# Kernel optimization log

Hardware: AMD Instinct MI355X
Metric: run time of the kernel (lower is better)

The kernel has to match this reference:

```python
import jax, jax.numpy as jnp
import numpy as np

D_MODEL = 1024
DEPTH = 1024

def setup_inputs() -> dict:
    key = jax.random.key(0)
    ks = jax.random.split(key, 7)
    scale = 1.0 / np.sqrt(D_MODEL)
    x = jax.random.normal(ks[0], (4, 2048, D_MODEL), dtype=jnp.float32)
    Wq = jax.random.normal(ks[1], (D_MODEL, DEPTH), dtype=jnp.float32) * scale
    Wk = jax.random.normal(ks[2], (D_MODEL, DEPTH), dtype=jnp.float32) * scale
    Wv = jax.random.normal(ks[3], (D_MODEL, DEPTH), dtype=jnp.float32) * scale
    bq = jnp.zeros((DEPTH,), dtype=jnp.float32)
    bk = jnp.zeros((DEPTH,), dtype=jnp.float32)
    bv = jnp.zeros((DEPTH,), dtype=jnp.float32)
    return {"x": x, "Wq": Wq, "bq": bq, "Wk": Wk, "bk": bk, "Wv": Wv, "bv": bv}

def reference(x, Wq, bq, Wk, bk, Wv, bv):
    # Q/K/V linear projections (Keras Dense: x @ W + b)
    q = jnp.einsum('bsd,de->bse', x, Wq) + bq  # [B,S,depth]
    k = jnp.einsum('bsd,de->bse', x, Wk) + bk
    v = jnp.einsum('bsd,de->bse', x, Wv) + bv
    d_k = jnp.asarray(q.shape[-1], dtype=q.dtype)
    scores = jnp.einsum('bse,bte->bst', q, k) / jnp.sqrt(d_k)  # [B,S,S]
    attn = jax.nn.softmax(scores, axis=-1)
    return jnp.einsum('bst,bte->bse', attn, v)  # [B,S,depth]
```

## Files before the change

kernel.cpp:

```cpp
#include <hip/hip_runtime.h>
#include <stdint.h>
#include <type_traits>

typedef unsigned short u16;
using short8  = __attribute__((ext_vector_type(8))) short;
using floatx4 = __attribute__((ext_vector_type(4))) float;

#define IC(n) (std::integral_constant<int, (n)>())

__device__ __forceinline__ u16 f2bf(float f) {
    unsigned u = __float_as_uint(f);
    u += 0x7fff + ((u >> 16) & 1);
    return (u16)(u >> 16);
}
__device__ __forceinline__ float bf2f(u16 h) {
    return __uint_as_float(((unsigned)h) << 16);
}

__device__ __forceinline__ void gload_lds16(const void* g, void* l) {
    auto gp = reinterpret_cast<const __attribute__((address_space(1))) unsigned int*>(
        reinterpret_cast<uintptr_t>(g));
    auto lp = reinterpret_cast<__attribute__((address_space(3))) unsigned int*>(
        reinterpret_cast<uintptr_t>(l));
    __builtin_amdgcn_global_load_lds(gp, lp, 16, 0, 0);
}

__global__ __launch_bounds__(256) void cvt_f32_bf16_kernel(
        const float* __restrict__ in, u16* __restrict__ out) {
    long i = ((long)blockIdx.x * 256 + threadIdx.x) * 4;
    float4 v = *(const float4*)(in + i);
    ushort4 o;
    o.x = f2bf(v.x); o.y = f2bf(v.y); o.z = f2bf(v.z); o.w = f2bf(v.w);
    *(ushort4*)(out + i) = o;
}

__global__ __launch_bounds__(256) void wt_kernel(
        const float* __restrict__ W0, const float* __restrict__ W1, const float* __restrict__ W2,
        u16* __restrict__ O0, u16* __restrict__ O1, u16* __restrict__ O2) {
    const float* W = blockIdx.z == 0 ? W0 : blockIdx.z == 1 ? W1 : W2;
    u16* O = blockIdx.z == 0 ? O0 : blockIdx.z == 1 ? O1 : O2;
    __shared__ float t[32][33];
    const int cx = threadIdx.x & 31, ry = threadIdx.x >> 5;
    const int d0 = blockIdx.x * 32, e0 = blockIdx.y * 32;
#pragma unroll
    for (int i = 0; i < 4; i++) t[ry + i * 8][cx] = W[(long)(d0 + ry + i * 8) * 1024 + e0 + cx];
    __syncthreads();
#pragma unroll
    for (int i = 0; i < 4; i++) O[(long)(e0 + ry + i * 8) * 1024 + d0 + cx] = f2bf(t[cx][ry + i * 8]);
}

__global__ __launch_bounds__(256) void vt_kernel(
        const u16* __restrict__ V, u16* __restrict__ Vt) {
    const int b = blockIdx.z;
    const u16* v = V + (long)b * 2048 * 1024;
    u16* o = Vt + (long)b * 1024 * 2048;
    __shared__ u16 t[32][33];
    const int cx = threadIdx.x & 31, ry = threadIdx.x >> 5;
    const int e0 = blockIdx.x * 32, t0 = blockIdx.y * 32;
#pragma unroll
    for (int i = 0; i < 4; i++) t[ry + i * 8][cx] = v[(long)(t0 + ry + i * 8) * 1024 + e0 + cx];
    __syncthreads();
#pragma unroll
    for (int i = 0; i < 4; i++) o[(long)(e0 + ry + i * 8) * 2048 + t0 + cx] = t[cx][ry + i * 8];
}

template <int MODE>
__global__ __launch_bounds__(512) void gemm8_kernel(
        const u16* __restrict__ A, const u16* __restrict__ Bt,
        void* __restrict__ out0, void* __restrict__ out1, void* __restrict__ out2,
        const float* __restrict__ b0, const float* __restrict__ b1, const float* __restrict__ b2,
        int K, int N, long sAb, long sBb, long sCb, float scale)
{
    extern __shared__ u16 lds[];
    const int tid = threadIdx.x, lane = tid & 63, wid = tid >> 6;
    const int wm = wid >> 2, wn = wid & 3;
    const int l15 = lane & 15, hib = (lane >> 4) * 16;

    const int nbx = gridDim.x;
    const int nwg = nbx * gridDim.y;
    int lin = blockIdx.y * nbx + blockIdx.x;
    lin = (lin & 7) * (nwg >> 3) + (lin >> 3);
    const long m0 = (long)(lin / nbx) * 256;
    const long n0 = (long)(lin % nbx) * 256;

    const u16* Ab = A + (long)blockIdx.z * sAb;
    const u16* Bb = Bt + (long)blockIdx.z * sBb;
    const long ldk = K;
    const int NT = K >> 6;

    auto stA = [&](int dbuf, int S, int kt) {
#pragma unroll
        for (int i = 0; i < 2; ++i) {
            const int rl = tid >> 3;
            const int R  = S * 64 + rl;
            const int cb = (tid & 7) * 16;
            const int scb = cb ^ ((R & 7) << 4);
            const u16* src = Ab + (m0 + i * 128 + R) * ldk + (long)kt * 64 + (scb >> 1);
            u16* dst = lds + dbuf * 32768 + i * 8192 + S * 4096 + wid * 512;
            gload_lds16(src, dst);
        }
    };
    auto stB = [&](int dbuf, int NHs, int kt) {
#pragma unroll
        for (int i = 0; i < 2; ++i) {
            const int c = i * 2 + (wid >> 2);
            const int h = c >> 1, rb = (c & 1) * 64;
            const int w = (wid & 3) * 64 + lane;
            const int r32 = w >> 3;
            const int R = rb + NHs * 32 + r32;
            const int cb = (w & 7) * 16;
            const int scb = cb ^ ((R & 7) << 4);
            const u16* src = Bb + (n0 + h * 128 + R) * ldk + (long)kt * 64 + (scb >> 1);
            u16* dst = lds + dbuf * 32768 + 16384 + h * 8192 + (rb + NHs * 32) * 64 + (wid & 3) * 512;
            gload_lds16(src, dst);
        }
    };

    floatx4 acc[8][4] = {};
    short8 afr[4][2], bfr[2][2];

    auto LA = [&](int dbuf, auto MHc) {
        constexpr int MH = decltype(MHc)::value;
        const char* reg = (const char*)(lds + dbuf * 32768 + wm * 8192);
#pragma unroll
        for (int fm = 0; fm < 4; ++fm)
#pragma unroll
            for (int ks = 0; ks < 2; ++ks) {
                const int r = MH * 64 + fm * 16 + l15;
                const int cb = ks * 64 + hib;
                afr[fm][ks] = *(const short8*)(reg + r * 128 + (cb ^ ((r & 7) << 4)));
            }
    };
    auto LB = [&](int dbuf, auto NHc) {
        constexpr int NH = decltype(NHc)::value;
        const char* reg = (const char*)(lds + dbuf * 32768 + 16384 + (wn >> 1) * 8192);
#pragma unroll
        for (int fn = 0; fn < 2; ++fn)
#pragma unroll
            for (int ks = 0; ks < 2; ++ks) {
                const int r = (wn & 1) * 64 + NH * 32 + fn * 16 + l15;
                const int cb = ks * 64 + hib;
                bfr[fn][ks] = *(const short8*)(reg + r * 128 + (cb ^ ((r & 7) << 4)));
            }
    };
    auto MM = [&](auto MHc, auto NHc) {
        constexpr int MH = decltype(MHc)::value;
        constexpr int NH = decltype(NHc)::value;
        __builtin_amdgcn_s_setprio(1);
#pragma unroll
        for (int fm = 0; fm < 4; ++fm)
#pragma unroll
            for (int fn = 0; fn < 2; ++fn)
#pragma unroll
                for (int ks = 0; ks < 2; ++ks)
                    acc[MH * 4 + fm][NH * 2 + fn] = __builtin_amdgcn_mfma_f32_16x16x32_bf16(
                        afr[fm][ks], bfr[fn][ks], acc[MH * 4 + fm][NH * 2 + fn], 0, 0, 0);
        __builtin_amdgcn_s_setprio(0);
    };

#define BAR()   __builtin_amdgcn_s_barrier()
#define WAIT0() asm volatile("s_waitcnt lgkmcnt(0)" ::: "memory")

    stA(0, 0, 0); stA(0, 1, 0); stB(0, 0, 0); stB(0, 1, 0);
    stA(1, 0, 1); stB(1, 1, 1); stA(1, 1, 1);
    asm volatile("s_waitcnt vmcnt(6)");
    BAR();

    auto pair = [&](auto LASTC, int kt0) {
        constexpr bool L = decltype(LASTC)::value;
        LA(0, IC(0)); LB(0, IC(0));
        stB(1, 0, kt0 + 1);
        asm volatile("s_waitcnt lgkmcnt(8)");
        BAR(); WAIT0(); MM(IC(0), IC(0)); BAR();
        LB(0, IC(1));
        if (!L) stA(0, 0, kt0 + 2);
        BAR(); WAIT0(); MM(IC(0), IC(1)); BAR();
        LA(0, IC(1));
        if (!L) stB(0, 1, kt0 + 2);
        BAR(); WAIT0(); MM(IC(1), IC(1)); BAR();
        LB(0, IC(0));
        if (!L) stA(0, 1, kt0 + 2);
        BAR(); WAIT0(); MM(IC(1), IC(0));
        if (L) asm volatile("s_waitcnt vmcnt(0)");
        else   asm volatile("s_waitcnt vmcnt(6)");
        BAR();
        LA(1, IC(0)); LB(1, IC(0));
        if (!L) stB(0, 0, kt0 + 2);
        asm volatile("s_waitcnt lgkmcnt(8)");
        BAR(); WAIT0(); MM(IC(0), IC(0)); BAR();
        LB(1, IC(1));
        if (!L) stA(1, 0, kt0 + 3);
        BAR(); WAIT0(); MM(IC(0), IC(1)); BAR();
        LA(1, IC(1));
        if (!L) stB(1, 1, kt0 + 3);
        BAR(); WAIT0(); MM(IC(1), IC(1)); BAR();
        LB(1, IC(0));
        if (!L) stA(1, 1, kt0 + 3);
        BAR(); WAIT0(); MM(IC(1), IC(0));
        if (L) asm volatile("s_waitcnt vmcnt(0)");
        else   asm volatile("s_waitcnt vmcnt(6)");
        BAR();
    };

    const int NITER = NT >> 1;
    int it = 0;
    for (; it < NITER - 1; ++it) pair(std::false_type{}, 2 * it);
    pair(std::true_type{}, 2 * it);

#undef BAR
#undef WAIT0

    const int cr = (lane >> 4) * 4, cc = l15;
    if (MODE == 0) {
        const int sel = (int)(n0 >> 10);
        u16* O = (u16*)(sel == 0 ? out0 : sel == 1 ? out1 : out2);
        const float* bias = sel == 0 ? b0 : sel == 1 ? b1 : b2;
        const long nc0 = n0 & 1023;
#pragma unroll
        for (int an = 0; an < 4; ++an) {
            const long col = nc0 + wn * 64 + an * 16 + cc;
            const float bvv = bias[col];
#pragma unroll
            for (int am = 0; am < 8; ++am) {
                const long row = m0 + wm * 128 + am * 16 + cr;
#pragma unroll
                for (int j = 0; j < 4; ++j)
                    O[(row + j) * 1024 + col] = f2bf(acc[am][an][j] + bvv);
            }
        }
    } else {
#pragma unroll
        for (int an = 0; an < 4; ++an) {
            const long col = n0 + wn * 64 + an * 16 + cc;
#pragma unroll
            for (int am = 0; am < 8; ++am) {
                const long row = m0 + wm * 128 + am * 16 + cr;
#pragma unroll
                for (int j = 0; j < 4; ++j) {
                    const long idx = (long)blockIdx.z * sCb + (row + j) * (long)N + col;
                    if (MODE == 1) ((u16*)out0)[idx] = f2bf(acc[am][an][j] * scale);
                    else           ((float*)out0)[idx] = acc[am][an][j];
                }
            }
        }
    }
}

__global__ __launch_bounds__(256) void softmax_kernel(u16* __restrict__ S) {
    u16* p = S + (long)blockIdx.x * 2048;
    const int tid = threadIdx.x;
    union { int4 q; u16 u[8]; } in;
    in.q = *(const int4*)(p + tid * 8);
    float v[8];
#pragma unroll
    for (int i = 0; i < 8; i++) v[i] = bf2f(in.u[i]);
    float mx = v[0];
#pragma unroll
    for (int i = 1; i < 8; i++) mx = fmaxf(mx, v[i]);
#pragma unroll
    for (int off = 32; off; off >>= 1) mx = fmaxf(mx, __shfl_xor(mx, off));
    __shared__ float red[8];
    if ((tid & 63) == 0) red[tid >> 6] = mx;
    __syncthreads();
    mx = fmaxf(fmaxf(red[0], red[1]), fmaxf(red[2], red[3]));
    float s = 0.f;
#pragma unroll
    for (int i = 0; i < 8; i++) { v[i] = __expf(v[i] - mx); s += v[i]; }
#pragma unroll
    for (int off = 32; off; off >>= 1) s += __shfl_xor(s, off);
    if ((tid & 63) == 0) red[4 + (tid >> 6)] = s;
    __syncthreads();
    s = red[4] + red[5] + red[6] + red[7];
    const float inv = 1.f / s;
    union { int4 q; u16 u[8]; } out;
#pragma unroll
    for (int i = 0; i < 8; i++) out.u[i] = f2bf(v[i] * inv);
    *(int4*)(p + tid * 8) = out.q;
}

extern "C" void kernel_launch(void* const* d_in, const int* in_sizes, int n_in,
                              void* d_out, int out_size, void* d_ws, size_t ws_size,
                              hipStream_t stream) {
    const float* x  = (const float*)d_in[0];
    const float* Wq = (const float*)d_in[1];
    const float* bq = (const float*)d_in[2];
    const float* Wk = (const float*)d_in[3];
    const float* bk = (const float*)d_in[4];
    const float* Wv = (const float*)d_in[5];
    const float* bv = (const float*)d_in[6];
    float* out = (float*)d_out;

    char* ws = (char*)d_ws;
    const long MB = 1L << 20;
    u16* xb = (u16*)(ws);
    u16* wt = (u16*)(ws + 16 * MB);
    u16* Q  = (u16*)(ws + 22 * MB);
    u16* Kb = (u16*)(ws + 38 * MB);
    u16* Vb = (u16*)(ws + 54 * MB);
    u16* Vt = (u16*)(ws + 70 * MB);
    u16* Sc = (u16*)(ws + 86 * MB);

    (void)hipFuncSetAttribute((const void*)gemm8_kernel<0>, hipFuncAttributeMaxDynamicSharedMemorySize, 131072);
    (void)hipFuncSetAttribute((const void*)gemm8_kernel<1>, hipFuncAttributeMaxDynamicSharedMemorySize, 131072);
    (void)hipFuncSetAttribute((const void*)gemm8_kernel<2>, hipFuncAttributeMaxDynamicSharedMemorySize, 131072);

    cvt_f32_bf16_kernel<<<8192, 256, 0, stream>>>(x, xb);
    wt_kernel<<<dim3(32, 32, 3), 256, 0, stream>>>(Wq, Wk, Wv, wt, wt + 1024 * 1024, wt + 2 * 1024 * 1024);
    gemm8_kernel<0><<<dim3(12, 32, 1), 512, 131072, stream>>>(
        xb, wt, Q, Kb, Vb, bq, bk, bv, 1024, 3072, 0, 0, 0, 1.f);
    vt_kernel<<<dim3(32, 64, 4), 256, 0, stream>>>(Vb, Vt);
    gemm8_kernel<1><<<dim3(8, 8, 4), 512, 131072, stream>>>(
        Q, Kb, Sc, nullptr, nullptr, nullptr, nullptr, nullptr,
        1024, 2048, 2048L * 1024, 2048L * 1024, 2048L * 2048, 0.03125f);
    softmax_kernel<<<8192, 256, 0, stream>>>(Sc);
    gemm8_kernel<2><<<dim3(4, 8, 4), 512, 131072, stream>>>(
        Sc, Vt, out, nullptr, nullptr, nullptr, nullptr, nullptr,
        2048, 1024, 2048L * 2048, 1024L * 2048, 2048L * 1024, 1.f);
}
```

Measured before the change: 198.6 us.

## Shrink GEMM tiles to 128x128, stage epilogue through LDS, vectorize V transpose

The three GEMMs move from 256x256 tiles with a finely interleaved 8-wave schedule to 128x128 tiles with a simpler double-buffered pipeline. LDS use drops to 64KB and the grids get four times as many workgroups. Epilogues now write through a swizzled LDS tile so global stores become 16-byte vectorized rows. The V transpose uses 64x64 tiles with ushort4 accesses. Smaller tiles improve occupancy and wave quantization but lower arithmetic intensity per tile and add global traffic.

```diff
diff --git a/kernel.cpp b/kernel.cpp
--- a/kernel.cpp
+++ b/kernel.cpp
@@ -4,6 +4,7 @@
 
 typedef unsigned short u16;
 using short8  = __attribute__((ext_vector_type(8))) short;
+using ushort8 = __attribute__((ext_vector_type(8))) unsigned short;
 using floatx4 = __attribute__((ext_vector_type(4))) float;
 
 #define IC(n) (std::integral_constant<int, (n)>())
@@ -54,14 +55,21 @@
     const int b = blockIdx.z;
     const u16* v = V + (long)b * 2048 * 1024;
     u16* o = Vt + (long)b * 1024 * 2048;
-    __shared__ u16 t[32][33];
-    const int cx = threadIdx.x & 31, ry = threadIdx.x >> 5;
-    const int e0 = blockIdx.x * 32, t0 = blockIdx.y * 32;
-#pragma unroll
-    for (int i = 0; i < 4; i++) t[ry + i * 8][cx] = v[(long)(t0 + ry + i * 8) * 1024 + e0 + cx];
-    __syncthreads();
-#pragma unroll
-    for (int i = 0; i < 4; i++) o[(long)(e0 + ry + i * 8) * 2048 + t0 + cx] = t[cx][ry + i * 8];
+    __shared__ u16 t[64][68];
+    const int c4 = (threadIdx.x & 15) * 4, r = threadIdx.x >> 4;
+    const int e0 = blockIdx.x * 64, t0 = blockIdx.y * 64;
+#pragma unroll
+    for (int i = 0; i < 4; i++)
+        *(ushort4*)&t[r + i * 16][c4] =
+            *(const ushort4*)(v + (long)(t0 + r + i * 16) * 1024 + e0 + c4);
+    __syncthreads();
+#pragma unroll
+    for (int i = 0; i < 4; i++) {
+        const int e = r + i * 16;
+        ushort4 d;
+        d.x = t[c4 + 0][e]; d.y = t[c4 + 1][e]; d.z = t[c4 + 2][e]; d.w = t[c4 + 3][e];
+        *(ushort4*)(o + (long)(e0 + e) * 2048 + t0 + c4) = d;
+    }
 }
 
 template <int MODE>
@@ -72,133 +80,107 @@
         int K, int N, long sAb, long sBb, long sCb, float scale)
 {
     extern __shared__ u16 lds[];
+    constexpr int DB = 16384;
     const int tid = threadIdx.x, lane = tid & 63, wid = tid >> 6;
-    const int wm = wid >> 2, wn = wid & 3;
+    const int wm = wid >> 1, wn = wid & 1;
     const int l15 = lane & 15, hib = (lane >> 4) * 16;
 
     const int nbx = gridDim.x;
     const int nwg = nbx * gridDim.y;
     int lin = blockIdx.y * nbx + blockIdx.x;
     lin = (lin & 7) * (nwg >> 3) + (lin >> 3);
-    const long m0 = (long)(lin / nbx) * 256;
-    const long n0 = (long)(lin % nbx) * 256;
+    const long m0 = (long)(lin / nbx) * 128;
+    const long n0 = (long)(lin % nbx) * 128;
 
     const u16* Ab = A + (long)blockIdx.z * sAb;
     const u16* Bb = Bt + (long)blockIdx.z * sBb;
     const long ldk = K;
     const int NT = K >> 6;
 
-    auto stA = [&](int dbuf, int S, int kt) {
+    auto stA = [&](int dbuf, int kt) {
 #pragma unroll
         for (int i = 0; i < 2; ++i) {
-            const int rl = tid >> 3;
-            const int R  = S * 64 + rl;
+            const int R  = i * 64 + (tid >> 3);
             const int cb = (tid & 7) * 16;
             const int scb = cb ^ ((R & 7) << 4);
-            const u16* src = Ab + (m0 + i * 128 + R) * ldk + (long)kt * 64 + (scb >> 1);
-            u16* dst = lds + dbuf * 32768 + i * 8192 + S * 4096 + wid * 512;
+            const u16* src = Ab + (m0 + R) * ldk + (long)kt * 64 + (scb >> 1);
+            u16* dst = lds + dbuf * DB + i * 4096 + tid * 8;
             gload_lds16(src, dst);
         }
     };
-    auto stB = [&](int dbuf, int NHs, int kt) {
+    auto stB = [&](int dbuf, int kt) {
 #pragma unroll
         for (int i = 0; i < 2; ++i) {
-            const int c = i * 2 + (wid >> 2);
-            const int h = c >> 1, rb = (c & 1) * 64;
-            const int w = (wid & 3) * 64 + lane;
-            const int r32 = w >> 3;
-            const int R = rb + NHs * 32 + r32;
-            const int cb = (w & 7) * 16;
+            const int R  = i * 64 + (tid >> 3);
+            const int cb = (tid & 7) * 16;
             const int scb = cb ^ ((R & 7) << 4);
-            const u16* src = Bb + (n0 + h * 128 + R) * ldk + (long)kt * 64 + (scb >> 1);
-            u16* dst = lds + dbuf * 32768 + 16384 + h * 8192 + (rb + NHs * 32) * 64 + (wid & 3) * 512;
+            const u16* src = Bb + (n0 + R) * ldk + (long)kt * 64 + (scb >> 1);
+            u16* dst = lds + dbuf * DB + 8192 + i * 4096 + tid * 8;
             gload_lds16(src, dst);
         }
     };
 
-    floatx4 acc[8][4] = {};
-    short8 afr[4][2], bfr[2][2];
-
-    auto LA = [&](int dbuf, auto MHc) {
-        constexpr int MH = decltype(MHc)::value;
-        const char* reg = (const char*)(lds + dbuf * 32768 + wm * 8192);
-#pragma unroll
-        for (int fm = 0; fm < 4; ++fm)
+    floatx4 acc[2][4] = {};
+    short8 a[2][2], b[4][2];
+
+    auto LA = [&](int dbuf) {
+        const char* reg = (const char*)(lds + dbuf * DB);
+#pragma unroll
+        for (int fm = 0; fm < 2; ++fm)
 #pragma unroll
             for (int ks = 0; ks < 2; ++ks) {
-                const int r = MH * 64 + fm * 16 + l15;
+                const int r = wm * 32 + fm * 16 + l15;
                 const int cb = ks * 64 + hib;
-                afr[fm][ks] = *(const short8*)(reg + r * 128 + (cb ^ ((r & 7) << 4)));
-            }
-    };
-    auto LB = [&](int dbuf, auto NHc) {
-        constexpr int NH = decltype(NHc)::value;
-        const char* reg = (const char*)(lds + dbuf * 32768 + 16384 + (wn >> 1) * 8192);
-#pragma unroll
-        for (int fn = 0; fn < 2; ++fn)
+                a[fm][ks] = *(const short8*)(reg + r * 128 + (cb ^ ((r & 7) << 4)));
+            }
+    };
+    auto LB = [&](int dbuf) {
+        const char* reg = (const char*)(lds + dbuf * DB + 8192);
+#pragma unroll
+        for (int fn = 0; fn < 4; ++fn)
 #pragma unroll
             for (int ks = 0; ks < 2; ++ks) {
-                const int r = (wn & 1) * 64 + NH * 32 + fn * 16 + l15;
+                const int r = wn * 64 + fn * 16 + l15;
                 const int cb = ks * 64 + hib;
-                bfr[fn][ks] = *(const short8*)(reg + r * 128 + (cb ^ ((r & 7) << 4)));
-            }
-    };
-    auto MM = [&](auto MHc, auto NHc) {
-        constexpr int MH = decltype(MHc)::value;
-        constexpr int NH = decltype(NHc)::value;
+                b[fn][ks] = *(const short8*)(reg + r * 128 + (cb ^ ((r & 7) << 4)));
+            }
+    };
+    auto MM = [&](auto FMc) {
+        constexpr int FM = decltype(FMc)::value;
         __builtin_amdgcn_s_setprio(1);
 #pragma unroll
-        for (int fm = 0; fm < 4; ++fm)
-#pragma unroll
-            for (int fn = 0; fn < 2; ++fn)
-#pragma unroll
-                for (int ks = 0; ks < 2; ++ks)
-                    acc[MH * 4 + fm][NH * 2 + fn] = __builtin_amdgcn_mfma_f32_16x16x32_bf16(
-                        afr[fm][ks], bfr[fn][ks], acc[MH * 4 + fm][NH * 2 + fn], 0, 0, 0);
+        for (int ks = 0; ks < 2; ++ks)
+#pragma unroll
+            for (int fn = 0; fn < 4; ++fn)
+                acc[FM][fn] = __builtin_amdgcn_mfma_f32_16x16x32_bf16(
+                    a[FM][ks], b[fn][ks], acc[FM][fn], 0, 0, 0);
         __builtin_amdgcn_s_setprio(0);
     };
 
-#define BAR()   __builtin_amdgcn_s_barrier()
-#define WAIT0() asm volatile("s_waitcnt lgkmcnt(0)" ::: "memory")
-
-    stA(0, 0, 0); stA(0, 1, 0); stB(0, 0, 0); stB(0, 1, 0);
-    stA(1, 0, 1); stB(1, 1, 1); stA(1, 1, 1);
-    asm volatile("s_waitcnt vmcnt(6)");
+#define BAR() __builtin_amdgcn_s_barrier()
+
+    stA(0, 0); stB(0, 0);
+    stA(1, 1);
+    asm volatile("s_waitcnt vmcnt(2)");
     BAR();
 
     auto pair = [&](auto LASTC, int kt0) {
         constexpr bool L = decltype(LASTC)::value;
-        LA(0, IC(0)); LB(0, IC(0));
-        stB(1, 0, kt0 + 1);
-        asm volatile("s_waitcnt lgkmcnt(8)");
-        BAR(); WAIT0(); MM(IC(0), IC(0)); BAR();
-        LB(0, IC(1));
-        if (!L) stA(0, 0, kt0 + 2);
-        BAR(); WAIT0(); MM(IC(0), IC(1)); BAR();
-        LA(0, IC(1));
-        if (!L) stB(0, 1, kt0 + 2);
-        BAR(); WAIT0(); MM(IC(1), IC(1)); BAR();
-        LB(0, IC(0));
-        if (!L) stA(0, 1, kt0 + 2);
-        BAR(); WAIT0(); MM(IC(1), IC(0));
+        stB(1, kt0 + 1);
+        LA(0); LB(0);
+        BAR(); MM(IC(0)); BAR();
+        if (!L) stA(0, kt0 + 2);
+        BAR(); MM(IC(1));
         if (L) asm volatile("s_waitcnt vmcnt(0)");
-        else   asm volatile("s_waitcnt vmcnt(6)");
+        else   asm volatile("s_waitcnt vmcnt(2)");
         BAR();
-        LA(1, IC(0)); LB(1, IC(0));
-        if (!L) stB(0, 0, kt0 + 2);
-        asm volatile("s_waitcnt lgkmcnt(8)");
-        BAR(); WAIT0(); MM(IC(0), IC(0)); BAR();
-        LB(1, IC(1));
-        if (!L) stA(1, 0, kt0 + 3);
-        BAR(); WAIT0(); MM(IC(0), IC(1)); BAR();
-        LA(1, IC(1));
-        if (!L) stB(1, 1, kt0 + 3);
-        BAR(); WAIT0(); MM(IC(1), IC(1)); BAR();
-        LB(1, IC(0));
-        if (!L) stA(1, 1, kt0 + 3);
-        BAR(); WAIT0(); MM(IC(1), IC(0));
+        if (!L) stB(0, kt0 + 2);
+        LA(1); LB(1);
+        BAR(); MM(IC(0)); BAR();
+        if (!L) stA(1, kt0 + 3);
+        BAR(); MM(IC(1));
         if (L) asm volatile("s_waitcnt vmcnt(0)");
-        else   asm volatile("s_waitcnt vmcnt(6)");
+        else   asm volatile("s_waitcnt vmcnt(2)");
         BAR();
     };
 
@@ -208,39 +190,66 @@
     pair(std::true_type{}, 2 * it);
 
 #undef BAR
-#undef WAIT0
 
     const int cr = (lane >> 4) * 4, cc = l15;
-    if (MODE == 0) {
-        const int sel = (int)(n0 >> 10);
-        u16* O = (u16*)(sel == 0 ? out0 : sel == 1 ? out1 : out2);
-        const float* bias = sel == 0 ? b0 : sel == 1 ? b1 : b2;
+    char* ldsB = (char*)lds;
+    __syncthreads();
+    if (MODE == 2) {
+#pragma unroll
+        for (int fn = 0; fn < 4; ++fn) {
+            const int col = wn * 64 + fn * 16 + cc;
+#pragma unroll
+            for (int fm = 0; fm < 2; ++fm) {
+                const int row = wm * 32 + fm * 16 + cr;
+#pragma unroll
+                for (int j = 0; j < 4; ++j)
+                    *(float*)(ldsB + ((((row + j) * 128 + col) * 4) ^ (((row + j) & 7) << 4))) =
+                        acc[fm][fn][j];
+            }
+        }
+        __syncthreads();
+        float* O = (float*)out0 + (long)blockIdx.z * sCb;
+#pragma unroll
+        for (int i = 0; i < 8; ++i) {
+            const int g4 = tid + i * 512;
+            const int row = g4 >> 5;
+            const int c4  = g4 & 31;
+            float4 v = *(const float4*)(ldsB + ((g4 * 16) ^ ((row & 7) << 4)));
+            *(float4*)(O + (m0 + row) * (long)N + n0 + c4 * 4) = v;
+        }
+    } else {
+        const int sel = (MODE == 0) ? (int)(n0 >> 10) : 0;
+        const float* bias = (MODE == 0) ? (sel == 0 ? b0 : sel == 1 ? b1 : b2) : nullptr;
         const long nc0 = n0 & 1023;
 #pragma unroll
-        for (int an = 0; an < 4; ++an) {
-            const long col = nc0 + wn * 64 + an * 16 + cc;
-            const float bvv = bias[col];
-#pragma unroll
-            for (int am = 0; am < 8; ++am) {
-                const long row = m0 + wm * 128 + am * 16 + cr;
-#pragma unroll
-                for (int j = 0; j < 4; ++j)
-                    O[(row + j) * 1024 + col] = f2bf(acc[am][an][j] + bvv);
-            }
-        }
-    } else {
-#pragma unroll
-        for (int an = 0; an < 4; ++an) {
-            const long col = n0 + wn * 64 + an * 16 + cc;
-#pragma unroll
-            for (int am = 0; am < 8; ++am) {
-                const long row = m0 + wm * 128 + am * 16 + cr;
+        for (int fn = 0; fn < 4; ++fn) {
+            const int col = wn * 64 + fn * 16 + cc;
+            const float bvv = (MODE == 0) ? bias[nc0 + col] : 0.f;
+#pragma unroll
+            for (int fm = 0; fm < 2; ++fm) {
+                const int row = wm * 32 + fm * 16 + cr;
 #pragma unroll
                 for (int j = 0; j < 4; ++j) {
-                    const long idx = (long)blockIdx.z * sCb + (row + j) * (long)N + col;
-                    if (MODE == 1) ((u16*)out0)[idx] = f2bf(acc[am][an][j] * scale);
-                    else           ((float*)out0)[idx] = acc[am][an][j];
+                    float v = acc[fm][fn][j];
+                    if (MODE == 1) v *= scale;
+                    v += bvv;
+                    *(u16*)(ldsB + ((((row + j) * 128 + col) * 2) ^ (((row + j) & 7) << 4))) = f2bf(v);
                 }
+            }
+        }
+        __syncthreads();
+#pragma unroll
+        for (int i = 0; i < 4; ++i) {
+            const int g8 = tid + i * 512;
+            const int row = g8 >> 4;
+            const int c8  = g8 & 15;
+            ushort8 v = *(const ushort8*)(ldsB + ((g8 * 16) ^ ((row & 7) << 4)));
+            if (MODE == 0) {
+                u16* O = (u16*)(sel == 0 ? out0 : sel == 1 ? out1 : out2);
+                *(ushort8*)(O + (m0 + row) * 1024 + nc0 + c8 * 8) = v;
+            } else {
+                u16* O = (u16*)out0 + (long)blockIdx.z * sCb;
+                *(ushort8*)(O + (m0 + row) * (long)N + n0 + c8 * 8) = v;
             }
         }
     }
@@ -300,20 +309,20 @@
     u16* Vt = (u16*)(ws + 70 * MB);
     u16* Sc = (u16*)(ws + 86 * MB);
 
-    (void)hipFuncSetAttribute((const void*)gemm8_kernel<0>, hipFuncAttributeMaxDynamicSharedMemorySize, 131072);
-    (void)hipFuncSetAttribute((const void*)gemm8_kernel<1>, hipFuncAttributeMaxDynamicSharedMemorySize, 131072);
-    (void)hipFuncSetAttribute((const void*)gemm8_kernel<2>, hipFuncAttributeMaxDynamicSharedMemorySize, 131072);
+    (void)hipFuncSetAttribute((const void*)gemm8_kernel<0>, hipFuncAttributeMaxDynamicSharedMemorySize, 65536);
+    (void)hipFuncSetAttribute((const void*)gemm8_kernel<1>, hipFuncAttributeMaxDynamicSharedMemorySize, 65536);
+    (void)hipFuncSetAttribute((const void*)gemm8_kernel<2>, hipFuncAttributeMaxDynamicSharedMemorySize, 65536);
 
     cvt_f32_bf16_kernel<<<8192, 256, 0, stream>>>(x, xb);
     wt_kernel<<<dim3(32, 32, 3), 256, 0, stream>>>(Wq, Wk, Wv, wt, wt + 1024 * 1024, wt + 2 * 1024 * 1024);
-    gemm8_kernel<0><<<dim3(12, 32, 1), 512, 131072, stream>>>(
+    gemm8_kernel<0><<<dim3(24, 64, 1), 512, 65536, stream>>>(
         xb, wt, Q, Kb, Vb, bq, bk, bv, 1024, 3072, 0, 0, 0, 1.f);
-    vt_kernel<<<dim3(32, 64, 4), 256, 0, stream>>>(Vb, Vt);
-    gemm8_kernel<1><<<dim3(8, 8, 4), 512, 131072, stream>>>(
+    vt_kernel<<<dim3(16, 32, 4), 256, 0, stream>>>(Vb, Vt);
+    gemm8_kernel<1><<<dim3(16, 16, 4), 512, 65536, stream>>>(
         Q, Kb, Sc, nullptr, nullptr, nullptr, nullptr, nullptr,
         1024, 2048, 2048L * 1024, 2048L * 1024, 2048L * 2048, 0.03125f);
     softmax_kernel<<<8192, 256, 0, stream>>>(Sc);
-    gemm8_kernel<2><<<dim3(4, 8, 4), 512, 131072, stream>>>(
+    gemm8_kernel<2><<<dim3(8, 16, 4), 512, 65536, stream>>>(
         Sc, Vt, out, nullptr, nullptr, nullptr, nullptr, nullptr,
         2048, 1024, 2048L * 2048, 1024L * 2048, 2048L * 1024, 1.f);
 }
```

After: 197.1 us. No clear change (-0.8%).
